# Kernel tuning notes

Hardware: AMD Instinct MI355X
Metric: run time of the kernel (lower is better)

## Reference

```python
import jax, jax.numpy as jnp
import numpy as np

C = 1024          # channels
RED = 16          # reduction
RC = C // RED     # 64 bottleneck channels
BZ, NUM_PROPS = 4, 256
BP = BZ * NUM_PROPS


def setup_inputs() -> dict:
    key = jax.random.key(0)
    ks = jax.random.split(key, 10)
    x_props = jax.random.normal(ks[0], (BP, C, 7, 7), dtype=jnp.float32)
    x_query = jax.random.normal(ks[1], (BZ, C, 8, 8), dtype=jnp.float32)
    s_conv = 1.0 / np.sqrt(C)   # kaiming-uniform-ish for conv1d 1x1 (fan_in=C)
    s_mlp = 1.0 / np.sqrt(RC)   # Linear fan_in = RC
    pc_w = jax.random.uniform(ks[2], (RC, C), minval=-s_conv, maxval=s_conv)
    pc_b = jax.random.uniform(ks[3], (RC,), minval=-s_conv, maxval=s_conv)
    qc_w = jax.random.uniform(ks[4], (RC, C), minval=-s_conv, maxval=s_conv)
    qc_b = jax.random.uniform(ks[5], (RC,), minval=-s_conv, maxval=s_conv)
    pm_w = jax.random.uniform(ks[6], (C, RC), minval=-s_mlp, maxval=s_mlp)
    pm_b = jax.random.uniform(ks[7], (C,), minval=-s_mlp, maxval=s_mlp)
    qm_w = jax.random.uniform(ks[8], (C, RC), minval=-s_mlp, maxval=s_mlp)
    qm_b = jax.random.uniform(ks[9], (C,), minval=-s_mlp, maxval=s_mlp)
    return {"x_props": x_props, "x_query": x_query,
            "pc_w": pc_w, "pc_b": pc_b, "qc_w": qc_w, "qc_b": qc_b,
            "pm_w": pm_w, "pm_b": pm_b, "qm_w": qm_w, "qm_b": qm_b}


def reference(x_props, x_query, pc_w, pc_b, qc_w, qc_b, pm_w, pm_b, qm_w, qm_b):
    bp, c, hp, wp = x_props.shape
    bz, _, hq, wq = x_query.shape
    n = bp // bz
    L = hp * wp
    # bilinear resize (half-pixel centers == torch align_corners=False)
    r_query = jax.image.resize(x_query, (bz, c, hp, wp), method='bilinear')
    # 1x1 conv bottlenecks (conv1d over flattened spatial dim)
    q_feat = jnp.einsum('rc,bcl->brl', qc_w, r_query.reshape(bz, c, L)) + qc_b[None, :, None]   # [bz, RC, L]
    p_feat = jnp.einsum('rc,bcl->brl', pc_w, x_props.reshape(bp, c, L)) + pc_b[None, :, None]   # [bp, RC, L]
    # similarity contracts spatial dim; query feature shared across props of same image
    p_feat_g = p_feat.reshape(bz, n, -1, L)
    sim = jnp.einsum('bnrl,bsl->bnrs', p_feat_g, q_feat)                                        # [bz, n, RC, RC]
    p_rel = sim.mean(axis=3).reshape(bp, -1)                                                    # [bp, RC]
    q_rel = sim.mean(axis=2).reshape(bp, -1)                                                    # [bp, RC]
    # channel-gate MLPs
    p_att = jax.nn.sigmoid(p_rel @ pm_w.T + pm_b)                                               # [bp, C]
    q_att = jax.nn.sigmoid(q_rel @ qm_w.T + qm_b)                                               # [bp, C]
    # co-excitation
    f_props = x_props * p_att[:, :, None, None]
    xq_rep = jnp.broadcast_to(x_query[:, None], (bz, n, c, hq, wq)).reshape(bp, c, hq, wq)
    f_query = xq_rep * q_att[:, :, None, None]
    return f_props, f_query, p_att.reshape(bp, c, 1, 1)
```

## Files before the change

### kernel.cpp

```cpp
#include <hip/hip_runtime.h>


typedef float v4f __attribute__((ext_vector_type(4)));

#define WQBAR  0
#define WPCBW  320
#define WPCBB  1344
#define WQF    1408
#define WPMBF  14336
#define WQMBF  47104

#define OUT_FP 0
#define OUT_FQ 51380224
#define OUT_PA 118489088

__device__ __forceinline__ float sigmoidf(float v) {
    return 1.0f / (1.0f + __expf(-v));
}
__device__ __forceinline__ unsigned short bf16_rne(float x) {
    unsigned u = __float_as_uint(x);
    return (unsigned short)((u + 0x7FFFu + ((u >> 16) & 1u)) >> 16);
}
__device__ __forceinline__ unsigned div49(unsigned e) {
    return __umulhi(e, 2804876602u) >> 5;
}

__global__ __launch_bounds__(1024) void k_prepall(
    const float* __restrict__ xq, const float* __restrict__ qc_w,
    const float* __restrict__ qc_b, const float* __restrict__ pc_w,
    const float* __restrict__ pc_b, const float* __restrict__ pm_w,
    const float* __restrict__ qm_w, float* __restrict__ ws)
{
    const int blk = blockIdx.x, t = threadIdx.x;
    if (blk < 196) {
        __shared__ float rq[1024];
        __shared__ float qf_s[64];
        const int b = blk / 49, l = blk - b * 49;
        const int wave = t >> 6, lane = t & 63;
        const int i = l / 7, j = l - i * 7;
        float fi = (2 * i + 1) * (1.0f / 14.0f);
        float fj = (2 * j + 1) * (1.0f / 14.0f);
        float wi0 = (1.0f - 0.875f * fi) * (1.0f / 1.125f); float wi1 = 1.0f - wi0;
        float wj0 = (1.0f - 0.875f * fj) * (1.0f / 1.125f); float wj1 = 1.0f - wj0;
        const float* X = xq + ((size_t)(b * 1024 + t) << 6);
        rq[t] = wi0 * (wj0 * X[i * 8 + j]       + wj1 * X[i * 8 + j + 1])
              + wi1 * (wj0 * X[(i + 1) * 8 + j] + wj1 * X[(i + 1) * 8 + j + 1]);
        __syncthreads();
        #pragma unroll
        for (int ii = 0; ii < 4; ++ii) {
            int s = wave * 4 + ii;
            const float* wr = qc_w + s * 1024;
            float part = 0.0f;
            #pragma unroll
            for (int k = 0; k < 16; ++k) part += wr[k * 64 + lane] * rq[k * 64 + lane];
            #pragma unroll
            for (int off = 32; off; off >>= 1) part += __shfl_down(part, off, 64);
            if (lane == 0) {
                float val = part + qc_b[s];
                ws[WQF + b * 3136 + s * 49 + l] = val;
                qf_s[s] = val;
            }
        }
        __syncthreads();
        if (t == 0) {
            float s = 0.0f;
            #pragma unroll
            for (int k = 0; k < 64; ++k) s += qf_s[k];
            ws[WQBAR + b * 49 + l] = s * (1.0f / 64.0f);
        }
    } else if (blk == 196) {
        float s = 0.0f;
        for (int r = 0; r < 64; ++r) s += pc_w[r * 1024 + t];
        ws[WPCBW + t] = s * (1.0f / 64.0f);
        if (t == 0) {
            float sb = 0.0f;
            for (int r = 0; r < 64; ++r) sb += pc_b[r];
            ws[WPCBB] = sb * (1.0f / 64.0f);
        }
    } else {
        int idx = (blk - 197) * 1024 + t;
        int r = (idx & 65535) >> 10, c = idx & 1023;
        float w = (idx < 65536) ? pm_w[c * 64 + r] : qm_w[c * 64 + r];
        unsigned short* dst = (unsigned short*)(ws + (idx < 65536 ? WPMBF : WQMBF));
        dst[idx & 65535] = bf16_rne(w);
    }
}

__global__ __launch_bounds__(256) void k_main(
    const float* __restrict__ x, const float* __restrict__ xq,
    const float* __restrict__ pc_w, const float* __restrict__ pc_b,
    const float* __restrict__ pm_b, const float* __restrict__ qm_b,
    float* __restrict__ ws, float* __restrict__ patt_out,
    float* __restrict__ fprops, float* __restrict__ fquery)
{
    __shared__ float xs[6272];
    __shared__ float y_s[1024];
    __shared__ float pcb_s[1024];
    __shared__ float qbar_s[49];
    __shared__ float sq_s;
    __shared__ float pbar_part[2][49];
    __shared__ float pbar_s[49];
    __shared__ float prel_s[64];
    __shared__ float qrel_s[64];

    const int t = threadIdx.x, wave = t >> 6, lane = t & 63;
    const int p = blockIdx.x, b = p >> 8;

    if (t < 49) qbar_s[t] = ws[WQBAR + b * 49 + t];
    for (int k = t; k < 1024; k += 256) pcb_s[k] = ws[WPCBW + k];
    const float pcbarb = ws[WPCBB];

    const float4* xp4 = (const float4*)(x + (size_t)p * 50176);
    float pbar_acc = 0.0f;

    for (int ch = 0; ch < 8; ++ch) {
        __syncthreads();
        const float4* src = xp4 + ch * 1568;
        float4* xs4 = (float4*)xs;
        for (int k = t; k < 1568; k += 256) xs4[k] = src[k];
        __syncthreads();
        if (ch == 0 && t == 0) {
            float s = 0.0f;
            #pragma unroll
            for (int l = 0; l < 49; ++l) s += qbar_s[l];
            sq_s = s;
        }
        if (wave < 2) {
            int c = wave * 64 + lane;
            const float* row = xs + c * 49;
            float acc = 0.0f;
            #pragma unroll
            for (int l = 0; l < 49; ++l) acc += row[l] * qbar_s[l];
            y_s[ch * 128 + c] = acc;
        } else if (lane < 49) {
            int cw = (wave - 2) * 64;
            const float* base = xs + cw * 49 + lane;
            const float* pw = pcb_s + ch * 128 + cw;
            float a = 0.0f;
            #pragma unroll
            for (int c = 0; c < 64; ++c) a += pw[c] * base[c * 49];
            pbar_acc += a;
        }
    }
    if (wave >= 2 && lane < 49) pbar_part[wave - 2][lane] = pbar_acc;
    __syncthreads();
    if (t < 49) pbar_s[t] = pbar_part[0][t] + pbar_part[1][t] + pcbarb;
    __syncthreads();
    const float sumqbar = sq_s;

    #pragma unroll
    for (int i = 0; i < 16; ++i) {
        int r = wave * 16 + i;
        const float* wr = pc_w + r * 1024;
        float part = 0.0f;
        #pragma unroll
        for (int k = 0; k < 16; ++k) part += wr[k * 64 + lane] * y_s[k * 64 + lane];
        #pragma unroll
        for (int off = 32; off; off >>= 1) part += __shfl_down(part, off, 64);
        if (lane == 0) prel_s[r] = part + pc_b[r] * sumqbar;
    }
    if (t < 64) {
        const float* qfr = ws + WQF + (b * 3136 + t * 49);
        float a = 0.0f;
        #pragma unroll
        for (int l = 0; l < 49; ++l) a += pbar_s[l] * qfr[l];
        qrel_s[t] = a;
    }
    __syncthreads();

    {
        const unsigned* wp = (const unsigned*)(ws + WPMBF);
        const unsigned* wq = (const unsigned*)(ws + WQMBF);
        float4 ap = {0, 0, 0, 0}, aq = {0, 0, 0, 0};
        #pragma unroll
        for (int r = 0; r < 64; ++r) {
            float pr = prel_s[r], qr = qrel_s[r];
            unsigned p01 = wp[r * 512 + 2 * t];
            unsigned p23 = wp[r * 512 + 2 * t + 1];
            ap.x += __uint_as_float(p01 << 16) * pr;
            ap.y += __uint_as_float(p01 & 0xFFFF0000u) * pr;
            ap.z += __uint_as_float(p23 << 16) * pr;
            ap.w += __uint_as_float(p23 & 0xFFFF0000u) * pr;
            unsigned q01 = wq[r * 512 + 2 * t];
            unsigned q23 = wq[r * 512 + 2 * t + 1];
            aq.x += __uint_as_float(q01 << 16) * qr;
            aq.y += __uint_as_float(q01 & 0xFFFF0000u) * qr;
            aq.z += __uint_as_float(q23 << 16) * qr;
            aq.w += __uint_as_float(q23 & 0xFFFF0000u) * qr;
        }
        float4 pb = ((const float4*)pm_b)[t];
        float4 qb = ((const float4*)qm_b)[t];
        float4 po, qo;
        po.x = sigmoidf(ap.x + pb.x); po.y = sigmoidf(ap.y + pb.y);
        po.z = sigmoidf(ap.z + pb.z); po.w = sigmoidf(ap.w + pb.w);
        qo.x = sigmoidf(aq.x + qb.x); qo.y = sigmoidf(aq.y + qb.y);
        qo.z = sigmoidf(aq.z + qb.z); qo.w = sigmoidf(aq.w + qb.w);
        ((float4*)patt_out)[p * 256 + t] = po;
        __syncthreads();
        ((float4*)y_s)[t]   = po;
        ((float4*)pcb_s)[t] = qo;
    }
    __syncthreads();

    {
        const v4f* xg4 = (const v4f*)(x + (size_t)p * 50176);
        v4f* fp4 = (v4f*)(fprops + (size_t)p * 50176);
        for (int i = 0; i < 49; ++i) {
            int k = i * 256 + t;
            unsigned e = 4u * (unsigned)k;
            unsigned c0 = div49(e);
            unsigned m = e - 49u * c0;
            float a0 = y_s[c0];
            float a1 = y_s[c0 + (m >= 46u)];
            v4f v = xg4[k];
            v4f g;
            g.x = a0;
            g.y = (m >= 48u) ? a1 : a0;
            g.z = (m >= 47u) ? a1 : a0;
            g.w = (m >= 46u) ? a1 : a0;
            __builtin_nontemporal_store(v * g, fp4 + k);
        }
    }

    {
        const v4f* xq4 = (const v4f*)(xq + ((size_t)b << 16));
        v4f* fq4 = (v4f*)(fquery + ((size_t)p << 16));
        for (int i = 0; i < 64; ++i) {
            int k = i * 256 + t;
            float att = pcb_s[k >> 4];
            v4f v = xq4[k];
            __builtin_nontemporal_store(v * att, fq4 + k);
        }
    }
}

extern "C" void kernel_launch(void* const* d_in, const int* in_sizes, int n_in,
                              void* d_out, int out_size, void* d_ws, size_t ws_size,
                              hipStream_t stream) {
    const float* x_props = (const float*)d_in[0];
    const float* x_query = (const float*)d_in[1];
    const float* pc_w    = (const float*)d_in[2];
    const float* pc_b    = (const float*)d_in[3];
    const float* qc_w    = (const float*)d_in[4];
    const float* qc_b    = (const float*)d_in[5];
    const float* pm_w    = (const float*)d_in[6];
    const float* pm_b    = (const float*)d_in[7];
    const float* qm_w    = (const float*)d_in[8];
    const float* qm_b    = (const float*)d_in[9];
    float* out = (float*)d_out;
    float* ws  = (float*)d_ws;

    k_prepall<<<325, 1024, 0, stream>>>(x_query, qc_w, qc_b, pc_w, pc_b, pm_w, qm_w, ws);
    k_main<<<1024, 256, 0, stream>>>(x_props, x_query, pc_w, pc_b, pm_b, qm_b, ws,
                                     out + OUT_PA, out + OUT_FP, out + OUT_FQ);
}
```

Measured before the change: 160.1 us.

## Double-buffer proposal tile loads and rebalance pbar reduction across waves

The staging loop now loads 16 smaller chunks (64 channels) into two alternating LDS buffers, prefetching the next chunk into registers while computing on the current one. This halves the syncs per chunk and overlaps global loads with compute. The pbar work moves to three waves (22/21/21 channels) while wave 0 does the qbar dot for 64 channels. The gating loop also replaces the per-iteration div49 with an incremental channel/remainder update. The register prefetch raises register use, and the pbar inner loop is no longer unrolled.

```diff
diff --git a/kernel.cpp b/kernel.cpp
--- a/kernel.cpp
+++ b/kernel.cpp
@@ -98,7 +98,7 @@
     __shared__ float pcb_s[1024];
     __shared__ float qbar_s[49];
     __shared__ float sq_s;
-    __shared__ float pbar_part[2][49];
+    __shared__ float pbar_part[3][49];
     __shared__ float pbar_s[49];
     __shared__ float prel_s[64];
     __shared__ float qrel_s[64];
@@ -111,40 +111,60 @@
     const float pcbarb = ws[WPCBB];
 
     const float4* xp4 = (const float4*)(x + (size_t)p * 50176);
+    float4* xs4 = (float4*)xs;
+
+    const int poff = (wave == 1) ? 0 : (wave == 2) ? 22 : 43;
+    const int pcnt = (wave == 1) ? 22 : 21;
     float pbar_acc = 0.0f;
 
-    for (int ch = 0; ch < 8; ++ch) {
-        __syncthreads();
-        const float4* src = xp4 + ch * 1568;
-        float4* xs4 = (float4*)xs;
-        for (int k = t; k < 1568; k += 256) xs4[k] = src[k];
-        __syncthreads();
-        if (ch == 0 && t == 0) {
+    {
+        const float4* src = xp4;
+        float4 r0 = src[t], r1 = src[t + 256], r2 = src[t + 512];
+        float4 r3;
+        if (t < 16) r3 = src[t + 768];
+        xs4[t] = r0; xs4[t + 256] = r1; xs4[t + 512] = r2;
+        if (t < 16) xs4[t + 768] = r3;
+    }
+    __syncthreads();
+
+    for (int g = 0; g < 16; ++g) {
+        float4 r0, r1, r2, r3;
+        if (g < 15) {
+            const float4* src = xp4 + (g + 1) * 784;
+            r0 = src[t]; r1 = src[t + 256]; r2 = src[t + 512];
+            if (t < 16) r3 = src[t + 768];
+        }
+        if (g == 0 && t == 0) {
             float s = 0.0f;
             #pragma unroll
             for (int l = 0; l < 49; ++l) s += qbar_s[l];
             sq_s = s;
         }
-        if (wave < 2) {
-            int c = wave * 64 + lane;
-            const float* row = xs + c * 49;
+        const float* xb = xs + (g & 1) * 3136;
+        if (wave == 0) {
+            const float* row = xb + lane * 49;
             float acc = 0.0f;
             #pragma unroll
             for (int l = 0; l < 49; ++l) acc += row[l] * qbar_s[l];
-            y_s[ch * 128 + c] = acc;
+            y_s[g * 64 + lane] = acc;
         } else if (lane < 49) {
-            int cw = (wave - 2) * 64;
-            const float* base = xs + cw * 49 + lane;
-            const float* pw = pcb_s + ch * 128 + cw;
+            const float* base = xb + poff * 49 + lane;
+            const float* pw = pcb_s + g * 64 + poff;
             float a = 0.0f;
-            #pragma unroll
-            for (int c = 0; c < 64; ++c) a += pw[c] * base[c * 49];
+            for (int c = 0; c < pcnt; ++c) a += pw[c] * base[c * 49];
             pbar_acc += a;
         }
-    }
-    if (wave >= 2 && lane < 49) pbar_part[wave - 2][lane] = pbar_acc;
-    __syncthreads();
-    if (t < 49) pbar_s[t] = pbar_part[0][t] + pbar_part[1][t] + pcbarb;
+        if (g < 15) {
+            float* xw = xs + ((g + 1) & 1) * 3136;
+            float4* xw4 = (float4*)xw;
+            xw4[t] = r0; xw4[t + 256] = r1; xw4[t + 512] = r2;
+            if (t < 16) xw4[t + 768] = r3;
+        }
+        __syncthreads();
+    }
+    if (wave >= 1 && lane < 49) pbar_part[wave - 1][lane] = pbar_acc;
+    __syncthreads();
+    if (t < 49) pbar_s[t] = pbar_part[0][t] + pbar_part[1][t] + pbar_part[2][t] + pcbarb;
     __syncthreads();
     const float sumqbar = sq_s;
 
@@ -205,11 +225,11 @@
     {
         const v4f* xg4 = (const v4f*)(x + (size_t)p * 50176);
         v4f* fp4 = (v4f*)(fprops + (size_t)p * 50176);
+        unsigned e0 = 4u * (unsigned)t;
+        unsigned c0 = div49(e0);
+        unsigned m = e0 - 49u * c0;
         for (int i = 0; i < 49; ++i) {
             int k = i * 256 + t;
-            unsigned e = 4u * (unsigned)k;
-            unsigned c0 = div49(e);
-            unsigned m = e - 49u * c0;
             float a0 = y_s[c0];
             float a1 = y_s[c0 + (m >= 46u)];
             v4f v = xg4[k];
@@ -219,6 +239,8 @@
             g.z = (m >= 47u) ? a1 : a0;
             g.w = (m >= 46u) ? a1 : a0;
             __builtin_nontemporal_store(v * g, fp4 + k);
+            c0 += 20u; m += 44u;
+            if (m >= 49u) { m -= 49u; ++c0; }
         }
     }
 
```

Measured after the change: 156.8 us, median of 2. 2.1% less time.

## Double k_main block size to 512 threads and redistribute per-thread work

Applied to the files above, without the earlier changes.

Launches k_main with 512 threads instead of 256, splitting the pbar reduction across six waves, the p_rel rows across eight waves, and the gate MLP to two channels per thread. The output streaming loops now stride by 512 and update channel/offset indices incrementally instead of dividing by 49 each iteration. The aim is more memory-level parallelism per block and more waves in flight on this bandwidth-bound kernel. In exchange there is more synchronization cost per block and a launch_bounds hint of 8 blocks per unit that may constrain registers.

```diff
diff --git a/kernel.cpp b/kernel.cpp
--- a/kernel.cpp
+++ b/kernel.cpp
@@ -86,7 +86,7 @@
     }
 }
 
-__global__ __launch_bounds__(256) void k_main(
+__global__ __launch_bounds__(512, 8) void k_main(
     const float* __restrict__ x, const float* __restrict__ xq,
     const float* __restrict__ pc_w, const float* __restrict__ pc_b,
     const float* __restrict__ pm_b, const float* __restrict__ qm_b,
@@ -98,7 +98,7 @@
     __shared__ float pcb_s[1024];
     __shared__ float qbar_s[49];
     __shared__ float sq_s;
-    __shared__ float pbar_part[2][49];
+    __shared__ float pbar_part[6][49];
     __shared__ float pbar_s[49];
     __shared__ float prel_s[64];
     __shared__ float qrel_s[64];
@@ -107,17 +107,21 @@
     const int p = blockIdx.x, b = p >> 8;
 
     if (t < 49) qbar_s[t] = ws[WQBAR + b * 49 + t];
-    for (int k = t; k < 1024; k += 256) pcb_s[k] = ws[WPCBW + k];
+    for (int k = t; k < 1024; k += 512) pcb_s[k] = ws[WPCBW + k];
     const float pcbarb = ws[WPCBB];
 
     const float4* xp4 = (const float4*)(x + (size_t)p * 50176);
+
+    const int w6 = wave - 2;
+    const int poff = 21 * w6 + (w6 >= 1) + (w6 >= 4);
+    const int pcnt = 21 + (w6 == 0) + (w6 == 3);
     float pbar_acc = 0.0f;
 
     for (int ch = 0; ch < 8; ++ch) {
         __syncthreads();
         const float4* src = xp4 + ch * 1568;
         float4* xs4 = (float4*)xs;
-        for (int k = t; k < 1568; k += 256) xs4[k] = src[k];
+        for (int k = t; k < 1568; k += 512) xs4[k] = src[k];
         __syncthreads();
         if (ch == 0 && t == 0) {
             float s = 0.0f;
@@ -133,24 +137,27 @@
             for (int l = 0; l < 49; ++l) acc += row[l] * qbar_s[l];
             y_s[ch * 128 + c] = acc;
         } else if (lane < 49) {
-            int cw = (wave - 2) * 64;
-            const float* base = xs + cw * 49 + lane;
-            const float* pw = pcb_s + ch * 128 + cw;
+            const float* base = xs + poff * 49 + lane;
+            const float* pw = pcb_s + ch * 128 + poff;
             float a = 0.0f;
-            #pragma unroll
-            for (int c = 0; c < 64; ++c) a += pw[c] * base[c * 49];
+            for (int c = 0; c < pcnt; ++c) a += pw[c] * base[c * 49];
             pbar_acc += a;
         }
     }
     if (wave >= 2 && lane < 49) pbar_part[wave - 2][lane] = pbar_acc;
     __syncthreads();
-    if (t < 49) pbar_s[t] = pbar_part[0][t] + pbar_part[1][t] + pcbarb;
+    if (t < 49) {
+        float s = pcbarb;
+        #pragma unroll
+        for (int w = 0; w < 6; ++w) s += pbar_part[w][t];
+        pbar_s[t] = s;
+    }
     __syncthreads();
     const float sumqbar = sq_s;
 
     #pragma unroll
-    for (int i = 0; i < 16; ++i) {
-        int r = wave * 16 + i;
+    for (int i = 0; i < 8; ++i) {
+        int r = wave * 8 + i;
         const float* wr = pc_w + r * 1024;
         float part = 0.0f;
         #pragma unroll
@@ -171,45 +178,35 @@
     {
         const unsigned* wp = (const unsigned*)(ws + WPMBF);
         const unsigned* wq = (const unsigned*)(ws + WQMBF);
-        float4 ap = {0, 0, 0, 0}, aq = {0, 0, 0, 0};
-        #pragma unroll
+        float ap0 = 0.0f, ap1 = 0.0f, aq0 = 0.0f, aq1 = 0.0f;
+        #pragma unroll 16
         for (int r = 0; r < 64; ++r) {
             float pr = prel_s[r], qr = qrel_s[r];
-            unsigned p01 = wp[r * 512 + 2 * t];
-            unsigned p23 = wp[r * 512 + 2 * t + 1];
-            ap.x += __uint_as_float(p01 << 16) * pr;
-            ap.y += __uint_as_float(p01 & 0xFFFF0000u) * pr;
-            ap.z += __uint_as_float(p23 << 16) * pr;
-            ap.w += __uint_as_float(p23 & 0xFFFF0000u) * pr;
-            unsigned q01 = wq[r * 512 + 2 * t];
-            unsigned q23 = wq[r * 512 + 2 * t + 1];
-            aq.x += __uint_as_float(q01 << 16) * qr;
-            aq.y += __uint_as_float(q01 & 0xFFFF0000u) * qr;
-            aq.z += __uint_as_float(q23 << 16) * qr;
-            aq.w += __uint_as_float(q23 & 0xFFFF0000u) * qr;
-        }
-        float4 pb = ((const float4*)pm_b)[t];
-        float4 qb = ((const float4*)qm_b)[t];
-        float4 po, qo;
-        po.x = sigmoidf(ap.x + pb.x); po.y = sigmoidf(ap.y + pb.y);
-        po.z = sigmoidf(ap.z + pb.z); po.w = sigmoidf(ap.w + pb.w);
-        qo.x = sigmoidf(aq.x + qb.x); qo.y = sigmoidf(aq.y + qb.y);
-        qo.z = sigmoidf(aq.z + qb.z); qo.w = sigmoidf(aq.w + qb.w);
-        ((float4*)patt_out)[p * 256 + t] = po;
-        __syncthreads();
-        ((float4*)y_s)[t]   = po;
-        ((float4*)pcb_s)[t] = qo;
+            unsigned pw2 = wp[r * 512 + t];
+            unsigned qw2 = wq[r * 512 + t];
+            ap0 += __uint_as_float(pw2 << 16) * pr;
+            ap1 += __uint_as_float(pw2 & 0xFFFF0000u) * pr;
+            aq0 += __uint_as_float(qw2 << 16) * qr;
+            aq1 += __uint_as_float(qw2 & 0xFFFF0000u) * qr;
+        }
+        float2 pb = ((const float2*)pm_b)[t];
+        float2 qb = ((const float2*)qm_b)[t];
+        float2 po, qo;
+        po.x = sigmoidf(ap0 + pb.x); po.y = sigmoidf(ap1 + pb.y);
+        qo.x = sigmoidf(aq0 + qb.x); qo.y = sigmoidf(aq1 + qb.y);
+        ((float2*)patt_out)[p * 512 + t] = po;
+        ((float2*)y_s)[t]   = po;
+        ((float2*)pcb_s)[t] = qo;
     }
     __syncthreads();
 
     {
         const v4f* xg4 = (const v4f*)(x + (size_t)p * 50176);
         v4f* fp4 = (v4f*)(fprops + (size_t)p * 50176);
-        for (int i = 0; i < 49; ++i) {
-            int k = i * 256 + t;
-            unsigned e = 4u * (unsigned)k;
-            unsigned c0 = div49(e);
-            unsigned m = e - 49u * c0;
+        unsigned e0 = 4u * (unsigned)t;
+        unsigned c0 = div49(e0);
+        unsigned m = e0 - 49u * c0;
+        for (int k = t; k < 12544; k += 512) {
             float a0 = y_s[c0];
             float a1 = y_s[c0 + (m >= 46u)];
             v4f v = xg4[k];
@@ -219,14 +216,15 @@
             g.z = (m >= 47u) ? a1 : a0;
             g.w = (m >= 46u) ? a1 : a0;
             __builtin_nontemporal_store(v * g, fp4 + k);
+            c0 += 41u; m += 39u;
+            if (m >= 49u) { m -= 49u; ++c0; }
         }
     }
 
     {
         const v4f* xq4 = (const v4f*)(xq + ((size_t)b << 16));
         v4f* fq4 = (v4f*)(fquery + ((size_t)p << 16));
-        for (int i = 0; i < 64; ++i) {
-            int k = i * 256 + t;
+        for (int k = t; k < 16384; k += 512) {
             float att = pcb_s[k >> 4];
             v4f v = xq4[k];
             __builtin_nontemporal_store(v * att, fq4 + k);
@@ -251,6 +249,6 @@
     float* ws  = (float*)d_ws;
 
     k_prepall<<<325, 1024, 0, stream>>>(x_query, qc_w, qc_b, pc_w, pc_b, pm_w, qm_w, ws);
-    k_main<<<1024, 256, 0, stream>>>(x_props, x_query, pc_w, pc_b, pm_b, qm_b, ws,
+    k_main<<<1024, 512, 0, stream>>>(x_props, x_query, pc_w, pc_b, pm_b, qm_b, ws,
                                      out + OUT_PA, out + OUT_FP, out + OUT_FQ);
 }
```

Measured after the change: 161.9 us. About the same (+1.2%).
